# Kernel optimization log

Measured on AMD Instinct MI355X. Metric: run time of the kernel, lower is better.

## Reference

```python
import jax, jax.numpy as jnp
import numpy as np

B, S, D, H, DFF = 4, 2048, 1024, 16, 4096
HD = D // H  # head_dim = 64


def rmsnorm(x, scale, eps=1e-6):
    var = jnp.mean(jnp.square(x), axis=-1, keepdims=True)
    return x * jax.lax.rsqrt(var + eps) * scale


def setup_inputs() -> dict:
    key = jax.random.key(0)
    ks = jax.random.split(key, 16)
    s = 1.0 / np.sqrt(D)
    inp = {
        "x": jax.random.normal(ks[0], (B, S, D), jnp.float32),
        "wq": jax.random.normal(ks[1], (D, D), jnp.float32) * s,
        "bq": jnp.zeros((D,), jnp.float32),
        "wk": jax.random.normal(ks[2], (D, D), jnp.float32) * s,
        "bk": jnp.zeros((D,), jnp.float32),
        "wv": jax.random.normal(ks[3], (D, D), jnp.float32) * s,
        "bv": jnp.zeros((D,), jnp.float32),
        "wbeta": jax.random.normal(ks[4], (D, H), jnp.float32) * s,
        "bbeta": jnp.zeros((H,), jnp.float32),
        "wo": jax.random.normal(ks[5], (D, D), jnp.float32) * s,
        "bo": jnp.zeros((D,), jnp.float32),
        "w1": jax.random.normal(ks[6], (D, DFF), jnp.float32) * s,
        "b1": jnp.zeros((DFF,), jnp.float32),
        "w2": jax.random.normal(ks[7], (DFF, D), jnp.float32) * (1.0 / np.sqrt(DFF)),
        "b2": jnp.zeros((D,), jnp.float32),
        "ln1_scale": jnp.ones((D,), jnp.float32),
        "ln2_scale": jnp.ones((D,), jnp.float32),
    }
    return inp


def gdn_attention(x, wq, bq, wk, bk, wv, bv, wbeta, bbeta, wo, bo):
    b, s, _ = x.shape
    q = (x @ wq + bq).reshape(b, s, H, HD)
    k = (x @ wk + bk).reshape(b, s, H, HD)
    v = (x @ wv + bv).reshape(b, s, H, HD)
    k = k / (jnp.linalg.norm(k, axis=-1, keepdims=True) + 1e-6)
    beta = jax.nn.sigmoid(x @ wbeta + bbeta)[..., None]  # (b, s, H, 1)

    # time-major for scan: (s, b, H, ...)
    q = jnp.transpose(q, (1, 0, 2, 3))
    k = jnp.transpose(k, (1, 0, 2, 3))
    v = jnp.transpose(v, (1, 0, 2, 3))
    beta = jnp.transpose(beta, (1, 0, 2, 3))

    def _step(Sm, inputs):
        q_t, k_t, v_t, beta_t = inputs
        Sk = jnp.einsum('bhde,bhe->bhd', Sm, k_t)
        delta = v_t - Sk
        Sm = Sm + beta_t[..., None] * jnp.einsum('bhd,bhe->bhde', delta, k_t)
        o_t = jnp.einsum('bhde,bhe->bhd', Sm, q_t)
        return Sm, o_t

    S0 = jnp.zeros((b, H, HD, HD), x.dtype)
    _, outputs = jax.lax.scan(_step, S0, (q, k, v, beta))
    outputs = jnp.transpose(outputs, (1, 0, 2, 3)).reshape(b, s, D)
    return outputs @ wo + bo


def reference(x, wq, bq, wk, bk, wv, bv, wbeta, bbeta, wo, bo,
              w1, b1, w2, b2, ln1_scale, ln2_scale):
    residual = x
    h = rmsnorm(x, ln1_scale)
    h = gdn_attention(h, wq, bq, wk, bk, wv, bv, wbeta, bbeta, wo, bo)
    x = h + residual
    residual = x
    h = rmsnorm(x, ln2_scale)
    h = jax.nn.gelu(h @ w1 + b1) @ w2 + b2
    return h + residual
```

## Files before the change

kernel.cpp:

```cpp
#include <hip/hip_runtime.h>

#define DEV __device__ __forceinline__

typedef short bf16x8 __attribute__((ext_vector_type(8)));
typedef float f32x4 __attribute__((ext_vector_type(4)));
typedef unsigned int uint;

DEV unsigned short f2b(float f) {
    uint u = __float_as_uint(f);
    u += 0x7fffu + ((u >> 16) & 1u);
    return (unsigned short)(u >> 16);
}
DEV uint packbf2(float a, float b) { return (uint)f2b(a) | ((uint)f2b(b) << 16); }
DEV float b2f(unsigned short s) { return __uint_as_float(((uint)s) << 16); }
DEV float b2f_lo(uint u) { return __uint_as_float(u << 16); }
DEV float b2f_hi(uint u) { return __uint_as_float(u & 0xffff0000u); }

DEV void async_cp16(const void* g, void* l) {
    __builtin_amdgcn_global_load_lds(
        (const __attribute__((address_space(1))) unsigned int*)g,
        (__attribute__((address_space(3))) unsigned int*)l, 16, 0, 0);
}

DEV float quad_sum(float x) {
    x += __int_as_float(__builtin_amdgcn_update_dpp(0, __float_as_int(x), 0xB1, 0xF, 0xF, true));
    x += __int_as_float(__builtin_amdgcn_update_dpp(0, __float_as_int(x), 0x4E, 0xF, 0xF, true));
    return x;
}

DEV float gelu_f(float u) {
    float p = u + 0.044715f * u * u * u;
    float e = __expf(-1.5957691216f * p);
    return __fdividef(u, 1.f + e);
}

DEV void dec8(uint4 p, float* o) {
    o[0] = b2f_lo(p.x); o[1] = b2f_hi(p.x); o[2] = b2f_lo(p.y); o[3] = b2f_hi(p.y);
    o[4] = b2f_lo(p.z); o[5] = b2f_hi(p.z); o[6] = b2f_lo(p.w); o[7] = b2f_hi(p.w);
}

__global__ __launch_bounds__(256) void transpose_cast_k(
    const float* __restrict__ in, unsigned short* __restrict__ out, int K, int N)
{
    __shared__ float tile[32][33];
    const int k0 = blockIdx.x * 32, n0 = blockIdx.y * 32;
    const int tx = threadIdx.x & 31, ty = threadIdx.x >> 5;
#pragma unroll
    for (int i = 0; i < 32; i += 8) {
        int n = n0 + tx;
        tile[ty + i][tx] = (n < N) ? in[(size_t)(k0 + ty + i) * N + n] : 0.0f;
    }
    __syncthreads();
#pragma unroll
    for (int i = 0; i < 32; i += 8) {
        out[(size_t)(n0 + ty + i) * K + (k0 + tx)] = f2b(tile[tx][ty + i]);
    }
}

__global__ void build_bias_k(const float* __restrict__ bq, const float* __restrict__ bk,
                             const float* __restrict__ bv, const float* __restrict__ bb,
                             float* __restrict__ outb)
{
    int i = blockIdx.x * 256 + threadIdx.x;
    if (i >= 3328) return;
    float v = 0.f;
    if (i < 1024)      v = bq[i];
    else if (i < 2048) v = bk[i - 1024];
    else if (i < 3072) v = bv[i - 2048];
    else if (i < 3088) v = bb[i - 3072];
    outb[i] = v;
}

__global__ __launch_bounds__(256) void rmsnorm_cast_k(
    const float* __restrict__ x, const float* __restrict__ scale,
    unsigned short* __restrict__ out)
{
    const int row = blockIdx.x;
    const int t = threadIdx.x;
    const float4 v = *(const float4*)(x + (size_t)row * 1024 + t * 4);
    float ss = v.x * v.x + v.y * v.y + v.z * v.z + v.w * v.w;
#pragma unroll
    for (int off = 1; off < 64; off <<= 1) ss += __shfl_xor(ss, off);
    __shared__ float wsum[4];
    if ((t & 63) == 0) wsum[t >> 6] = ss;
    __syncthreads();
    const float tot = wsum[0] + wsum[1] + wsum[2] + wsum[3];
    const float inv = rsqrtf(tot * (1.0f / 1024.0f) + 1e-6f);
    const float4 sc = *(const float4*)(scale + t * 4);
    uint lo = (uint)f2b(v.x * inv * sc.x) | ((uint)f2b(v.y * inv * sc.y) << 16);
    uint hi = (uint)f2b(v.z * inv * sc.z) | ((uint)f2b(v.w * inv * sc.w) << 16);
    uint2 pkd; pkd.x = lo; pkd.y = hi;
    *(uint2*)(out + (size_t)row * 1024 + t * 4) = pkd;
}

template <bool GELU, bool GUARD>
__global__ __launch_bounds__(512, 2) void gemm256(
    const unsigned short* __restrict__ A, const unsigned short* __restrict__ BT,
    const float* __restrict__ bias, unsigned short* __restrict__ C,
    int Nstride, int Nreal, int K)
{
    __shared__ __align__(16) unsigned short As[4][256 * 32];
    __shared__ __align__(16) unsigned short Bs[4][256 * 32];
    const int tid = threadIdx.x;
    const int wid = tid >> 6;
    const int lane = tid & 63;
    const int l16 = lane & 15, quad = lane >> 4;
    const int wm = wid & 1, wn = wid >> 1;
    const int m0 = blockIdx.x << 8, n0 = blockIdx.y << 8;

    const int srow = (wid << 5) + (lane >> 2);
    const int scol = (lane & 3) << 3;
    const unsigned short* Ag = A + (size_t)(m0 + srow) * K + scol;
    const unsigned short* Bg = BT + (size_t)(n0 + srow) * K + scol;
    const size_t rstep16 = (size_t)16 * K;
    const int ldst = wid << 10;

    f32x4 acc[8][4];
#pragma unroll
    for (int i = 0; i < 8; i++)
#pragma unroll
        for (int j = 0; j < 4; j++) acc[i][j] = (f32x4)0.f;

    const int aoff = ((wm << 7) + l16) * 32 + (quad << 3);
    const int boff = ((wn << 6) + l16) * 32 + (quad << 3);

    const int nt = K >> 5;
    async_cp16(Ag, &As[0][ldst]);
    async_cp16(Ag + rstep16, &As[0][ldst + 512]);
    async_cp16(Bg, &Bs[0][ldst]);
    async_cp16(Bg + rstep16, &Bs[0][ldst + 512]);
    async_cp16(Ag + 32, &As[1][ldst]);
    async_cp16(Ag + 32 + rstep16, &As[1][ldst + 512]);
    async_cp16(Bg + 32, &Bs[1][ldst]);
    async_cp16(Bg + 32 + rstep16, &Bs[1][ldst + 512]);
    asm volatile("s_waitcnt vmcnt(4)" ::: "memory");
    __builtin_amdgcn_s_barrier();

    for (int tb = 0; tb < nt; tb += 4) {
#pragma unroll
        for (int u = 0; u < 4; ++u) {
            const int t = tb + u;
            const int pb = (u + 2) & 3;
            const bool st = (t + 2) < nt;
            const size_t kpre = (size_t)(t + 2) << 5;
            bf16x8 af[4], bfr[4];
#pragma unroll
            for (int mi = 0; mi < 4; mi++) af[mi] = *(const bf16x8*)&As[u][aoff + mi * 512];
#pragma unroll
            for (int ni = 0; ni < 4; ni++) bfr[ni] = *(const bf16x8*)&Bs[u][boff + ni * 512];
            if (st) {
                async_cp16(Ag + kpre, &As[pb][ldst]);
                async_cp16(Ag + kpre + rstep16, &As[pb][ldst + 512]);
            }
            __builtin_amdgcn_s_barrier();
            asm volatile("s_waitcnt lgkmcnt(0)" ::: "memory");
            __builtin_amdgcn_s_setprio(1);
#pragma unroll
            for (int mi = 0; mi < 4; mi++)
#pragma unroll
                for (int ni = 0; ni < 4; ni++)
                    acc[mi][ni] = __builtin_amdgcn_mfma_f32_16x16x32_bf16(af[mi], bfr[ni], acc[mi][ni], 0, 0, 0);
            __builtin_amdgcn_s_setprio(0);
            __builtin_amdgcn_s_barrier();
#pragma unroll
            for (int mi = 0; mi < 4; mi++) af[mi] = *(const bf16x8*)&As[u][aoff + (mi + 4) * 512];
            if (st) {
                async_cp16(Bg + kpre, &Bs[pb][ldst]);
                async_cp16(Bg + kpre + rstep16, &Bs[pb][ldst + 512]);
            }
            asm volatile("s_waitcnt vmcnt(4)" ::: "memory");
            __builtin_amdgcn_s_barrier();
            asm volatile("s_waitcnt lgkmcnt(0)" ::: "memory");
            __builtin_amdgcn_s_setprio(1);
#pragma unroll
            for (int mi = 0; mi < 4; mi++)
#pragma unroll
                for (int ni = 0; ni < 4; ni++)
                    acc[mi + 4][ni] = __builtin_amdgcn_mfma_f32_16x16x32_bf16(af[mi], bfr[ni], acc[mi + 4][ni], 0, 0, 0);
            __builtin_amdgcn_s_setprio(0);
            __builtin_amdgcn_s_barrier();
        }
    }

    float bv[4];
    const int ccol = n0 + (wn << 6) + l16;
#pragma unroll
    for (int ni = 0; ni < 4; ni++) bv[ni] = bias[ccol + ni * 16];
#pragma unroll
    for (int mi = 0; mi < 8; mi++) {
        const int row = m0 + (wm << 7) + mi * 16 + (quad << 2);
#pragma unroll
        for (int r = 0; r < 4; r++) {
            unsigned short* Crow = C + (size_t)(row + r) * Nstride + ccol;
#pragma unroll
            for (int ni = 0; ni < 4; ni++) {
                float v = acc[mi][ni][r] + bv[ni];
                if (GELU) v = gelu_f(v);
                if (!GUARD || (ccol + ni * 16) < Nreal) Crow[ni * 16] = f2b(v);
            }
        }
    }
}

template <int MODE>
__global__ __launch_bounds__(256) void gemm_bt(
    const unsigned short* __restrict__ A, const unsigned short* __restrict__ BT,
    const float* __restrict__ bias, const float* __restrict__ add,
    void* __restrict__ Cout, int N, int K)
{
    __shared__ unsigned short As[128 * 32];
    __shared__ unsigned short Bs[128 * 32];
    const int tid = threadIdx.x;
    const int wid = tid >> 6;
    const int lane = tid & 63;
    const int m0 = blockIdx.x * 128;
    const int n0 = blockIdx.y * 128;

    const int lrow = lane >> 2;
    const int lkw = (((lane & 3) ^ ((lane >> 3) & 3))) * 8;

    const unsigned short* Ag0 = A + (size_t)(m0 + wid * 16 + lrow) * K + lkw;
    const unsigned short* Ag1 = A + (size_t)(m0 + wid * 16 + 64 + lrow) * K + lkw;
    const unsigned short* Bg0 = BT + (size_t)(n0 + wid * 16 + lrow) * K + lkw;
    const unsigned short* Bg1 = BT + (size_t)(n0 + wid * 16 + 64 + lrow) * K + lkw;
    unsigned short* As0 = &As[(wid * 16) * 32];
    unsigned short* As1 = &As[(wid * 16 + 64) * 32];
    unsigned short* Bs0 = &Bs[(wid * 16) * 32];
    unsigned short* Bs1 = &Bs[(wid * 16 + 64) * 32];

    f32x4 acc[4][4];
#pragma unroll
    for (int i = 0; i < 4; i++)
#pragma unroll
        for (int j = 0; j < 4; j++) acc[i][j] = (f32x4)0.f;

    const int wm = (wid & 1) * 64;
    const int wn = (wid >> 1) * 64;
    const int l16 = lane & 15;
    const int quad = lane >> 4;
    const int koffs = (quad ^ ((l16 >> 1) & 3)) * 8;

    for (int k0 = 0; k0 < K; k0 += 32) {
        async_cp16(Ag0 + k0, As0);
        async_cp16(Ag1 + k0, As1);
        async_cp16(Bg0 + k0, Bs0);
        async_cp16(Bg1 + k0, Bs1);
        __syncthreads();
        bf16x8 af[4], bfv[4];
#pragma unroll
        for (int i = 0; i < 4; i++) af[i] = *(const bf16x8*)&As[(wm + i * 16 + l16) * 32 + koffs];
#pragma unroll
        for (int j = 0; j < 4; j++) bfv[j] = *(const bf16x8*)&Bs[(wn + j * 16 + l16) * 32 + koffs];
#pragma unroll
        for (int i = 0; i < 4; i++)
#pragma unroll
            for (int j = 0; j < 4; j++)
                acc[i][j] = __builtin_amdgcn_mfma_f32_16x16x32_bf16(af[i], bfv[j], acc[i][j], 0, 0, 0);
        __syncthreads();
    }

    if (MODE == 2 || MODE == 3) {
        float* ep = ((wid & 2) ? (float*)Bs : (float*)As) + (wid & 1) * 1024;
        const int rr = lane >> 2, cg = lane & 3;
        unsigned short* Cu = (unsigned short*)Cout;
#pragma unroll
        for (int i = 0; i < 4; i++) {
#pragma unroll
            for (int p = 0; p < 2; p++) {
#pragma unroll
                for (int jj = 0; jj < 2; jj++) {
                    const int j = 2 * p + jj;
                    const float bv = bias[n0 + wn + j * 16 + l16];
#pragma unroll
                    for (int r = 0; r < 4; r++) {
                        float v = acc[i][j][r] + bv;
                        if (MODE == 2) v = gelu_f(v);
                        ep[(jj * 16 + l16) * 17 + quad * 4 + r] = v;
                    }
                }
                __syncthreads();
                uint4 pk;
                float f[8];
#pragma unroll
                for (int m = 0; m < 8; m++) f[m] = ep[(cg * 8 + m) * 17 + rr];
                pk.x = packbf2(f[0], f[1]); pk.y = packbf2(f[2], f[3]);
                pk.z = packbf2(f[4], f[5]); pk.w = packbf2(f[6], f[7]);
                *(uint4*)(Cu + (size_t)(m0 + wm + i * 16 + rr) * N + (n0 + wn + p * 32 + cg * 8)) = pk;
                __syncthreads();
            }
        }
    } else {
#pragma unroll
        for (int j = 0; j < 4; j++) {
            const int cg2 = n0 + wn + j * 16 + l16;
            const float bv = bias[cg2];
#pragma unroll
            for (int i = 0; i < 4; i++) {
                const int rg0 = m0 + wm + i * 16 + quad * 4;
#pragma unroll
                for (int r = 0; r < 4; r++) {
                    size_t idx = (size_t)(rg0 + r) * N + cg2;
                    float v = acc[i][j][r] + bv;
                    if (MODE == 1) v += add[idx];
                    ((float*)Cout)[idx] = v;
                }
            }
        }
    }
}


__global__ __launch_bounds__(256) void gdn_prep(
    unsigned short* __restrict__ qkv, unsigned short* __restrict__ Wg,
    unsigned short* __restrict__ ZTg, unsigned short* __restrict__ KTg)
{
    const int chunk = blockIdx.x, bh = blockIdx.y;
    const int b = bh >> 4, h = bh & 15;
    __shared__ float Ks[64 * 68];
    __shared__ float Ws[64 * 65];
    __shared__ float Zs[64 * 65];
    __shared__ float Asl[64 * 65];
    __shared__ float bs[64];
    const int tid = threadIdx.x;
    const int t = tid >> 2, c = tid & 3;
    unsigned short* rowp = qkv + (size_t)(b * 2048 + chunk * 64 + t) * 3200;

    float kn[16];
    {
        uint4 ka = *(const uint4*)(rowp + 1024 + h * 64 + 16 * c);
        uint4 kb = *(const uint4*)(rowp + 1024 + h * 64 + 16 * c + 8);
        dec8(ka, kn); dec8(kb, kn + 8);
    }
    float ss = 0.f;
#pragma unroll
    for (int j = 0; j < 16; j++) ss += kn[j] * kn[j];
    ss = quad_sum(ss);
    const float inv = 1.f / (sqrtf(ss) + 1e-6f);
#pragma unroll
    for (int j = 0; j < 16; j++) kn[j] *= inv;
#pragma unroll
    for (int j = 0; j < 16; j++) Ks[t * 68 + 16 * c + j] = kn[j];
    {
        uint4 p0, p1;
        p0.x = packbf2(kn[0], kn[1]);  p0.y = packbf2(kn[2], kn[3]);
        p0.z = packbf2(kn[4], kn[5]);  p0.w = packbf2(kn[6], kn[7]);
        p1.x = packbf2(kn[8], kn[9]);  p1.y = packbf2(kn[10], kn[11]);
        p1.z = packbf2(kn[12], kn[13]); p1.w = packbf2(kn[14], kn[15]);
        *(uint4*)(rowp + 1024 + h * 64 + 16 * c) = p0;
        *(uint4*)(rowp + 1024 + h * 64 + 16 * c + 8) = p1;
    }
    if (c == 0) bs[t] = 1.f / (1.f + __expf(-b2f(rowp[3072 + h])));
    __syncthreads();

    const float beta = bs[t];
#pragma unroll
    for (int j = 0; j < 16; j++) Ws[t * 65 + 16 * c + j] = beta * kn[j];
    {
        float vv[16];
        uint4 va = *(const uint4*)(rowp + 2048 + h * 64 + 16 * c);
        uint4 vb = *(const uint4*)(rowp + 2048 + h * 64 + 16 * c + 8);
        dec8(va, vv); dec8(vb, vv + 8);
#pragma unroll
        for (int j = 0; j < 16; j++) Zs[t * 65 + 16 * c + j] = beta * vv[j];
    }
    __syncthreads();

    {
        const int tt = tid >> 4, sx = tid & 15;
        float dm[4][4];
#pragma unroll
        for (int i = 0; i < 4; i++)
#pragma unroll
            for (int j = 0; j < 4; j++) dm[i][j] = 0.f;
        for (int d = 0; d < 64; d++) {
            float kt[4], ksv[4];
#pragma unroll
            for (int i = 0; i < 4; i++) kt[i] = Ks[(4 * tt + i) * 68 + d];
#pragma unroll
            for (int j = 0; j < 4; j++) ksv[j] = Ks[(4 * sx + j) * 68 + d];
#pragma unroll
            for (int i = 0; i < 4; i++)
#pragma unroll
                for (int j = 0; j < 4; j++) dm[i][j] += kt[i] * ksv[j];
        }
#pragma unroll
        for (int i = 0; i < 4; i++)
#pragma unroll
            for (int j = 0; j < 4; j++) {
                int T = 4 * tt + i, S_ = 4 * sx + j;
                Asl[T * 65 + S_] = (S_ < T) ? bs[T] * dm[i][j] : 0.f;
            }
    }
    __syncthreads();

    {
        const int wid = tid >> 6, lane = tid & 63;
        for (int qi = 0; qi < 4; qi++) {
            if (qi > 0) {
                const int tb = qi * 16 + wid * 4;
                float aw[4], az[4];
#pragma unroll
                for (int i = 0; i < 4; i++) { aw[i] = Ws[(tb + i) * 65 + lane]; az[i] = Zs[(tb + i) * 65 + lane]; }
                for (int s = 0; s < qi * 16; s++) {
                    float wsv = Ws[s * 65 + lane], zsv = Zs[s * 65 + lane];
#pragma unroll
                    for (int i = 0; i < 4; i++) {
                        float a = Asl[(tb + i) * 65 + s];
                        aw[i] -= a * wsv; az[i] -= a * zsv;
                    }
                }
#pragma unroll
                for (int i = 0; i < 4; i++) { Ws[(tb + i) * 65 + lane] = aw[i]; Zs[(tb + i) * 65 + lane] = az[i]; }
            }
            __syncthreads();
            if (wid == 0) {
                for (int T = qi * 16; T < qi * 16 + 16; T++) {
                    float a_ = Ws[T * 65 + lane];
                    for (int s = qi * 16; s < T; s++) a_ -= Asl[T * 65 + s] * Ws[s * 65 + lane];
                    Ws[T * 65 + lane] = a_;
                }
            } else if (wid == 1) {
                for (int T = qi * 16; T < qi * 16 + 16; T++) {
                    float a_ = Zs[T * 65 + lane];
                    for (int s = qi * 16; s < T; s++) a_ -= Asl[T * 65 + s] * Zs[s * 65 + lane];
                    Zs[T * 65 + lane] = a_;
                }
            }
            __syncthreads();
        }
    }

    const size_t cbase = ((size_t)bh * 32 + chunk) * 4096;
    {
#pragma unroll
        for (int half = 0; half < 2; half++) {
            uint4 w4;
            w4.x = packbf2(Ws[t * 65 + 16 * c + half * 8 + 0], Ws[t * 65 + 16 * c + half * 8 + 1]);
            w4.y = packbf2(Ws[t * 65 + 16 * c + half * 8 + 2], Ws[t * 65 + 16 * c + half * 8 + 3]);
            w4.z = packbf2(Ws[t * 65 + 16 * c + half * 8 + 4], Ws[t * 65 + 16 * c + half * 8 + 5]);
            w4.w = packbf2(Ws[t * 65 + 16 * c + half * 8 + 6], Ws[t * 65 + 16 * c + half * 8 + 7]);
            *(uint4*)(Wg + cbase + (size_t)((2 * c + half) * 64 + t) * 8) = w4;
        }
    }
    {
        const int jj = tid >> 2, tq = tid & 3;
#pragma unroll
        for (int half = 0; half < 2; half++) {
            uint4 z4;
            int i0 = half * 8;
            z4.x = packbf2(Zs[(16 * tq + i0 + 0) * 65 + jj], Zs[(16 * tq + i0 + 1) * 65 + jj]);
            z4.y = packbf2(Zs[(16 * tq + i0 + 2) * 65 + jj], Zs[(16 * tq + i0 + 3) * 65 + jj]);
            z4.z = packbf2(Zs[(16 * tq + i0 + 4) * 65 + jj], Zs[(16 * tq + i0 + 5) * 65 + jj]);
            z4.w = packbf2(Zs[(16 * tq + i0 + 6) * 65 + jj], Zs[(16 * tq + i0 + 7) * 65 + jj]);
            *(uint4*)(ZTg + cbase + (size_t)((2 * tq + half) * 64 + jj) * 8) = z4;
        }
    }
    {
        const int dd = tid >> 2, tq = tid & 3;
#pragma unroll
        for (int half = 0; half < 2; half++) {
            uint4 k4;
            int i0 = half * 8;
            k4.x = packbf2(Ks[(16 * tq + i0 + 0) * 68 + dd], Ks[(16 * tq + i0 + 1) * 68 + dd]);
            k4.y = packbf2(Ks[(16 * tq + i0 + 2) * 68 + dd], Ks[(16 * tq + i0 + 3) * 68 + dd]);
            k4.z = packbf2(Ks[(16 * tq + i0 + 4) * 68 + dd], Ks[(16 * tq + i0 + 5) * 68 + dd]);
            k4.w = packbf2(Ks[(16 * tq + i0 + 6) * 68 + dd], Ks[(16 * tq + i0 + 7) * 68 + dd]);
            *(uint4*)(KTg + cbase + (size_t)((2 * tq + half) * 64 + dd) * 8) = k4;
        }
    }
}

__global__ __launch_bounds__(256, 1) void gdn_prop_mfma(
    const unsigned short* __restrict__ Wg, const unsigned short* __restrict__ KTg,
    const unsigned short* __restrict__ ZTg, unsigned short* __restrict__ Sall,
    unsigned short* __restrict__ Yg)
{
    const int bh = blockIdx.x;
    __shared__ unsigned short WbU[4096];
    __shared__ unsigned short KTbU[4096];
    __shared__ unsigned short ZTbU[4096];
    __shared__ unsigned short SbU[4096];
    const int tid = threadIdx.x;
    const int wid = tid >> 6;
    const int lane = tid & 63;
    const int l16 = lane & 15, quad = lane >> 4;

    f32x4 Sacc[4];
#pragma unroll
    for (int dt = 0; dt < 4; dt++) Sacc[dt] = (f32x4)0.f;

    for (int ch = 0; ch < 32; ch++) {
        const size_t cbase = ((size_t)bh * 32 + ch) * 4096;
#pragma unroll
        for (int p = 0; p < 2; p++) {
            const int n = wid * 2 + p;
            async_cp16(Wg + cbase + n * 512 + lane * 8, &WbU[n * 512]);
            async_cp16(KTg + cbase + n * 512 + lane * 8, &KTbU[n * 512]);
            async_cp16(ZTg + cbase + n * 512 + lane * 8, &ZTbU[n * 512]);
        }
#pragma unroll
        for (int dt = 0; dt < 4; dt++) {
#pragma unroll
            for (int r = 0; r < 4; r++) {
                const int j = wid * 16 + quad * 4 + r;
                SbU[((2 * dt + (l16 >> 3)) * 64 + j) * 8 + (l16 & 7)] = f2b(Sacc[dt][r]);
            }
            const int d = dt * 16 + l16;
            uint2 sp;
            sp.x = packbf2(Sacc[dt][0], Sacc[dt][1]);
            sp.y = packbf2(Sacc[dt][2], Sacc[dt][3]);
            *(uint2*)(Sall + cbase + d * 64 + wid * 16 + quad * 4) = sp;
        }
        __syncthreads();

        f32x4 t1[4];
#pragma unroll
        for (int tt = 0; tt < 4; tt++) t1[tt] = (f32x4)0.f;
#pragma unroll
        for (int kh = 0; kh < 2; kh++) {
            const int g = kh * 4 + quad;
            bf16x8 afr = *(const bf16x8*)&SbU[(g * 64 + wid * 16 + l16) * 8];
#pragma unroll
            for (int tt = 0; tt < 4; tt++) {
                bf16x8 bfr = *(const bf16x8*)&WbU[(g * 64 + tt * 16 + l16) * 8];
                t1[tt] = __builtin_amdgcn_mfma_f32_16x16x32_bf16(afr, bfr, t1[tt], 0, 0, 0);
            }
        }
#pragma unroll
        for (int tt = 0; tt < 4; tt++) {
            const int t = tt * 16 + l16;
            const int gb = (t >> 3) * 64;
            unsigned short ybf[4];
#pragma unroll
            for (int r = 0; r < 4; r++) {
                const int j = wid * 16 + quad * 4 + r;
                const float z = b2f(ZTbU[(gb + j) * 8 + (t & 7)]);
                ybf[r] = f2b(z - t1[tt][r]);
            }
#pragma unroll
            for (int r = 0; r < 4; r++) {
                const int j = wid * 16 + quad * 4 + r;
                ZTbU[(gb + j) * 8 + (t & 7)] = ybf[r];
            }
            uint2 yp;
            yp.x = (uint)ybf[0] | ((uint)ybf[1] << 16);
            yp.y = (uint)ybf[2] | ((uint)ybf[3] << 16);
            *(uint2*)(Yg + cbase + t * 64 + wid * 16 + quad * 4) = yp;
        }
#pragma unroll
        for (int kh = 0; kh < 2; kh++) {
            const int g = kh * 4 + quad;
            bf16x8 afr = *(const bf16x8*)&ZTbU[(g * 64 + wid * 16 + l16) * 8];
#pragma unroll
            for (int dt = 0; dt < 4; dt++) {
                bf16x8 bfr = *(const bf16x8*)&KTbU[(g * 64 + dt * 16 + l16) * 8];
                Sacc[dt] = __builtin_amdgcn_mfma_f32_16x16x32_bf16(afr, bfr, Sacc[dt], 0, 0, 0);
            }
        }
        __syncthreads();
    }
}

__global__ __launch_bounds__(256) void gdn_out(
    const unsigned short* __restrict__ qkv, const unsigned short* __restrict__ Yg,
    const unsigned short* __restrict__ Sall, unsigned short* __restrict__ attn)
{
    const int chunk = blockIdx.x, bh = blockIdx.y;
    const int b = bh >> 4, h = bh & 15;
    __shared__ float Qf[64 * 68];
    __shared__ float SfT[64 * 68];
    __shared__ float Ms[64 * 65];
    __shared__ uint Kp[64 * 33];
    __shared__ uint Yp[64 * 34];
    const int tid = threadIdx.x;
    const int t = tid >> 2, c = tid & 3;
    const size_t cbase = ((size_t)bh * 32 + chunk) * 4096;

    {
        const unsigned short* rowp = qkv + (size_t)(b * 2048 + chunk * 64 + t) * 3200;
        float qv[16];
        uint4 qa = *(const uint4*)(rowp + h * 64 + 16 * c);
        uint4 qb = *(const uint4*)(rowp + h * 64 + 16 * c + 8);
        dec8(qa, qv); dec8(qb, qv + 8);
#pragma unroll
        for (int m = 0; m < 16; m++) Qf[t * 68 + 16 * c + m] = qv[m];
        uint4 ka = *(const uint4*)(rowp + 1024 + h * 64 + 16 * c);
        uint4 kb = *(const uint4*)(rowp + 1024 + h * 64 + 16 * c + 8);
        Kp[t * 33 + 8 * c + 0] = ka.x; Kp[t * 33 + 8 * c + 1] = ka.y;
        Kp[t * 33 + 8 * c + 2] = ka.z; Kp[t * 33 + 8 * c + 3] = ka.w;
        Kp[t * 33 + 8 * c + 4] = kb.x; Kp[t * 33 + 8 * c + 5] = kb.y;
        Kp[t * 33 + 8 * c + 6] = kb.z; Kp[t * 33 + 8 * c + 7] = kb.w;
        const unsigned short* yrow = Yg + cbase + t * 64 + 16 * c;
        uint4 ya = *(const uint4*)yrow;
        uint4 yb = *(const uint4*)(yrow + 8);
        Yp[t * 34 + 8 * c + 0] = ya.x; Yp[t * 34 + 8 * c + 1] = ya.y;
        Yp[t * 34 + 8 * c + 2] = ya.z; Yp[t * 34 + 8 * c + 3] = ya.w;
        Yp[t * 34 + 8 * c + 4] = yb.x; Yp[t * 34 + 8 * c + 5] = yb.y;
        Yp[t * 34 + 8 * c + 6] = yb.z; Yp[t * 34 + 8 * c + 7] = yb.w;
        const unsigned short* srow = Sall + cbase + t * 64 + 16 * c;
        float sv[16];
        uint4 sa = *(const uint4*)srow;
        uint4 sb = *(const uint4*)(srow + 8);
        dec8(sa, sv); dec8(sb, sv + 8);
#pragma unroll
        for (int m = 0; m < 16; m++) SfT[t * 68 + 16 * c + m] = sv[m];
    }
    __syncthreads();

    const int tt = tid >> 4, sx = tid & 15;
    {
        float dm[4][4];
#pragma unroll
        for (int i = 0; i < 4; i++)
#pragma unroll
            for (int j = 0; j < 4; j++) dm[i][j] = 0.f;
        for (int p = 0; p < 32; p++) {
            float q0[4], q1[4];
#pragma unroll
            for (int i = 0; i < 4; i++) {
                q0[i] = Qf[(4 * tt + i) * 68 + 2 * p];
                q1[i] = Qf[(4 * tt + i) * 68 + 2 * p + 1];
            }
#pragma unroll
            for (int j = 0; j < 4; j++) {
                uint kp = Kp[(4 * sx + j) * 33 + p];
                float kk0 = b2f_lo(kp), kk1 = b2f_hi(kp);
#pragma unroll
                for (int i = 0; i < 4; i++) dm[i][j] += q0[i] * kk0 + q1[i] * kk1;
            }
        }
#pragma unroll
        for (int i = 0; i < 4; i++)
#pragma unroll
            for (int j = 0; j < 4; j++) {
                int T = 4 * tt + i, S_ = 4 * sx + j;
                Ms[T * 65 + S_] = (S_ <= T) ? dm[i][j] : 0.f;
            }
    }
    __syncthreads();

    {
        float o[4][4];
#pragma unroll
        for (int i = 0; i < 4; i++)
#pragma unroll
            for (int j = 0; j < 4; j++) o[i][j] = 0.f;
        for (int d = 0; d < 64; d++) {
            float qv[4];
#pragma unroll
            for (int i = 0; i < 4; i++) qv[i] = Qf[(4 * tt + i) * 68 + d];
#pragma unroll
            for (int j = 0; j < 4; j++) {
                float sv = SfT[d * 68 + 4 * sx + j];
#pragma unroll
                for (int i = 0; i < 4; i++) o[i][j] += qv[i] * sv;
            }
        }
        for (int s = 0; s < 64; s++) {
            float mv[4];
#pragma unroll
            for (int i = 0; i < 4; i++) mv[i] = Ms[(4 * tt + i) * 65 + s];
            uint2 yp2 = *(const uint2*)&Yp[s * 34 + 2 * sx];
            float yv0 = b2f_lo(yp2.x), yv1 = b2f_hi(yp2.x), yv2 = b2f_lo(yp2.y), yv3 = b2f_hi(yp2.y);
#pragma unroll
            for (int i = 0; i < 4; i++) {
                o[i][0] += mv[i] * yv0; o[i][1] += mv[i] * yv1;
                o[i][2] += mv[i] * yv2; o[i][3] += mv[i] * yv3;
            }
        }
#pragma unroll
        for (int i = 0; i < 4; i++) {
            uint2 op; op.x = packbf2(o[i][0], o[i][1]); op.y = packbf2(o[i][2], o[i][3]);
            *(uint2*)(attn + (size_t)(b * 2048 + chunk * 64 + 4 * tt + i) * 1024 + h * 64 + 4 * sx) = op;
        }
    }
}

static constexpr size_t OFF_H     = 0;
static constexpr size_t OFF_WQKVT = OFF_H + 16777216;
static constexpr size_t OFF_WOT   = OFF_WQKVT + 6553600;
static constexpr size_t OFF_W1T   = OFF_WOT + 2097152;
static constexpr size_t OFF_W2T   = OFF_W1T + 8388608;
static constexpr size_t OFF_BIAS  = OFF_W2T + 8388608;
static constexpr size_t OFF_QKV   = OFF_BIAS + 16384;
static constexpr size_t OFF_ATTN  = OFF_QKV + 67108864;
static constexpr size_t OFF_Y1    = OFF_ATTN + 16777216;
static constexpr size_t OFF_WG    = OFF_Y1 + 33554432;
static constexpr size_t OFF_YG    = OFF_WG + 16777216;

extern "C" void kernel_launch(void* const* d_in, const int* in_sizes, int n_in,
                              void* d_out, int out_size, void* d_ws, size_t ws_size,
                              hipStream_t stream)
{
    const float* x     = (const float*)d_in[0];
    const float* wq    = (const float*)d_in[1];
    const float* bq    = (const float*)d_in[2];
    const float* wk    = (const float*)d_in[3];
    const float* bk    = (const float*)d_in[4];
    const float* wv    = (const float*)d_in[5];
    const float* bv    = (const float*)d_in[6];
    const float* wbeta = (const float*)d_in[7];
    const float* bbeta = (const float*)d_in[8];
    const float* wo    = (const float*)d_in[9];
    const float* bo    = (const float*)d_in[10];
    const float* w1    = (const float*)d_in[11];
    const float* b1    = (const float*)d_in[12];
    const float* w2    = (const float*)d_in[13];
    const float* b2    = (const float*)d_in[14];
    const float* ln1   = (const float*)d_in[15];
    const float* ln2   = (const float*)d_in[16];

    char* ws = (char*)d_ws;
    unsigned short* hbuf  = (unsigned short*)(ws + OFF_H);
    unsigned short* Sall  = (unsigned short*)(ws + OFF_H);
    unsigned short* wqkvT = (unsigned short*)(ws + OFF_WG);
    unsigned short* woT   = (unsigned short*)(ws + OFF_WOT);
    unsigned short* w1T   = (unsigned short*)(ws + OFF_W1T);
    unsigned short* w2T   = (unsigned short*)(ws + OFF_W2T);
    float*          biasc = (float*)(ws + OFF_BIAS);
    unsigned short* qkvU  = (unsigned short*)(ws + OFF_QKV);
    unsigned short* gbuf  = (unsigned short*)(ws + OFF_QKV);
    unsigned short* attn  = (unsigned short*)(ws + OFF_ATTN);
    float*          y1    = (float*)(ws + OFF_Y1);
    unsigned short* ZTg   = (unsigned short*)(ws + OFF_Y1);
    unsigned short* KTg   = (unsigned short*)(ws + OFF_Y1 + 16777216);
    unsigned short* Wg    = (unsigned short*)(ws + OFF_WG);
    unsigned short* Yg    = (unsigned short*)(ws + OFF_YG);
    float*          out   = (float*)d_out;

    transpose_cast_k<<<dim3(32, 32), 256, 0, stream>>>(wq, wqkvT,               1024, 1024);
    transpose_cast_k<<<dim3(32, 32), 256, 0, stream>>>(wk, wqkvT + 1024 * 1024, 1024, 1024);
    transpose_cast_k<<<dim3(32, 32), 256, 0, stream>>>(wv, wqkvT + 2048 * 1024, 1024, 1024);
    transpose_cast_k<<<dim3(32, 8),  256, 0, stream>>>(wbeta, wqkvT + 3072 * 1024, 1024, 16);
    transpose_cast_k<<<dim3(32, 32), 256, 0, stream>>>(wo, woT, 1024, 1024);
    transpose_cast_k<<<dim3(32, 128), 256, 0, stream>>>(w1, w1T, 1024, 4096);
    transpose_cast_k<<<dim3(128, 32), 256, 0, stream>>>(w2, w2T, 4096, 1024);
    build_bias_k<<<13, 256, 0, stream>>>(bq, bk, bv, bbeta, biasc);

    rmsnorm_cast_k<<<8192, 256, 0, stream>>>(x, ln1, hbuf);
    gemm256<false, true><<<dim3(32, 13), 512, 0, stream>>>(hbuf, wqkvT, biasc, qkvU, 3200, 3200, 1024);
    gdn_prep<<<dim3(32, 64), 256, 0, stream>>>(qkvU, Wg, ZTg, KTg);
    gdn_prop_mfma<<<64, 256, 0, stream>>>(Wg, KTg, ZTg, Sall, Yg);
    gdn_out<<<dim3(32, 64), 256, 0, stream>>>(qkvU, Yg, Sall, attn);
    gemm_bt<1><<<dim3(64, 8), 256, 0, stream>>>(attn, woT, bo, x, y1, 1024, 1024);
    rmsnorm_cast_k<<<8192, 256, 0, stream>>>(y1, ln2, hbuf);
    gemm256<true, false><<<dim3(32, 16), 512, 0, stream>>>(hbuf, w1T, b1, gbuf, 4096, 4096, 1024);
    gemm_bt<1><<<dim3(64, 8), 256, 0, stream>>>(gbuf, w2T, b2, y1, out, 1024, 4096);
}
```

Baseline: 684.3 us.

## Replace gemm_bt with pipelined 128x256 GEMM and swizzle gemm256 LDS

The single-buffered 128x128 gemm_bt used for the output projection and FFN down-projection is replaced by a new 512-thread 128x256 kernel. It uses a 4-stage async global-to-LDS pipeline with prefetch two tiles ahead, fewer barriers, and raised wave priority around the MFMAs. gemm256 gains an XOR swizzle of the LDS K offset to reduce bank conflicts, and its last iterations now drain outstanding loads with vmcnt(0). The aim is to overlap memory with MFMA and improve reuse in the two K-heavy fp32-output GEMMs, at the cost of more LDS and a smaller grid of 256 blocks.

```diff
diff --git a/kernel.cpp b/kernel.cpp
--- a/kernel.cpp
+++ b/kernel.cpp
@@ -5,6 +5,10 @@
 typedef short bf16x8 __attribute__((ext_vector_type(8)));
 typedef float f32x4 __attribute__((ext_vector_type(4)));
 typedef unsigned int uint;
+
+#define SBAR()   asm volatile("s_barrier" ::: "memory")
+#define WAITV(n) asm volatile("s_waitcnt vmcnt(" #n ")" ::: "memory")
+#define WAITL()  asm volatile("s_waitcnt lgkmcnt(0)" ::: "memory")
 
 DEV unsigned short f2b(float f) {
     uint u = __float_as_uint(f);
@@ -109,7 +113,7 @@
     const int m0 = blockIdx.x << 8, n0 = blockIdx.y << 8;
 
     const int srow = (wid << 5) + (lane >> 2);
-    const int scol = (lane & 3) << 3;
+    const int scol = ((lane & 3) ^ ((lane >> 3) & 3)) << 3;
     const unsigned short* Ag = A + (size_t)(m0 + srow) * K + scol;
     const unsigned short* Bg = BT + (size_t)(n0 + srow) * K + scol;
     const size_t rstep16 = (size_t)16 * K;
@@ -121,8 +125,9 @@
 #pragma unroll
         for (int j = 0; j < 4; j++) acc[i][j] = (f32x4)0.f;
 
-    const int aoff = ((wm << 7) + l16) * 32 + (quad << 3);
-    const int boff = ((wn << 6) + l16) * 32 + (quad << 3);
+    const int ksw = (quad ^ ((l16 >> 1) & 3)) << 3;
+    const int aoff = ((wm << 7) + l16) * 32 + ksw;
+    const int boff = ((wn << 6) + l16) * 32 + ksw;
 
     const int nt = K >> 5;
     async_cp16(Ag, &As[0][ldst]);
@@ -133,8 +138,8 @@
     async_cp16(Ag + 32 + rstep16, &As[1][ldst + 512]);
     async_cp16(Bg + 32, &Bs[1][ldst]);
     async_cp16(Bg + 32 + rstep16, &Bs[1][ldst + 512]);
-    asm volatile("s_waitcnt vmcnt(4)" ::: "memory");
-    __builtin_amdgcn_s_barrier();
+    WAITV(4);
+    SBAR();
 
     for (int tb = 0; tb < nt; tb += 4) {
 #pragma unroll
@@ -152,8 +157,8 @@
                 async_cp16(Ag + kpre, &As[pb][ldst]);
                 async_cp16(Ag + kpre + rstep16, &As[pb][ldst + 512]);
             }
-            __builtin_amdgcn_s_barrier();
-            asm volatile("s_waitcnt lgkmcnt(0)" ::: "memory");
+            SBAR();
+            WAITL();
             __builtin_amdgcn_s_setprio(1);
 #pragma unroll
             for (int mi = 0; mi < 4; mi++)
@@ -161,16 +166,18 @@
                 for (int ni = 0; ni < 4; ni++)
                     acc[mi][ni] = __builtin_amdgcn_mfma_f32_16x16x32_bf16(af[mi], bfr[ni], acc[mi][ni], 0, 0, 0);
             __builtin_amdgcn_s_setprio(0);
-            __builtin_amdgcn_s_barrier();
+            SBAR();
 #pragma unroll
             for (int mi = 0; mi < 4; mi++) af[mi] = *(const bf16x8*)&As[u][aoff + (mi + 4) * 512];
             if (st) {
                 async_cp16(Bg + kpre, &Bs[pb][ldst]);
                 async_cp16(Bg + kpre + rstep16, &Bs[pb][ldst + 512]);
-            }
-            asm volatile("s_waitcnt vmcnt(4)" ::: "memory");
-            __builtin_amdgcn_s_barrier();
-            asm volatile("s_waitcnt lgkmcnt(0)" ::: "memory");
+                WAITV(4);
+            } else {
+                WAITV(0);
+            }
+            SBAR();
+            WAITL();
             __builtin_amdgcn_s_setprio(1);
 #pragma unroll
             for (int mi = 0; mi < 4; mi++)
@@ -178,7 +185,7 @@
                 for (int ni = 0; ni < 4; ni++)
                     acc[mi + 4][ni] = __builtin_amdgcn_mfma_f32_16x16x32_bf16(af[mi], bfr[ni], acc[mi + 4][ni], 0, 0, 0);
             __builtin_amdgcn_s_setprio(0);
-            __builtin_amdgcn_s_barrier();
+            SBAR();
         }
     }
 
@@ -202,31 +209,29 @@
     }
 }
 
-template <int MODE>
-__global__ __launch_bounds__(256) void gemm_bt(
+template <bool ADD>
+__global__ __launch_bounds__(512, 2) void gemm128n256(
     const unsigned short* __restrict__ A, const unsigned short* __restrict__ BT,
     const float* __restrict__ bias, const float* __restrict__ add,
-    void* __restrict__ Cout, int N, int K)
-{
-    __shared__ unsigned short As[128 * 32];
-    __shared__ unsigned short Bs[128 * 32];
+    float* __restrict__ C, int N, int K)
+{
+    __shared__ __align__(16) unsigned short As[4][128 * 32];
+    __shared__ __align__(16) unsigned short Bs[4][256 * 32];
     const int tid = threadIdx.x;
     const int wid = tid >> 6;
     const int lane = tid & 63;
-    const int m0 = blockIdx.x * 128;
-    const int n0 = blockIdx.y * 128;
-
-    const int lrow = lane >> 2;
-    const int lkw = (((lane & 3) ^ ((lane >> 3) & 3))) * 8;
-
-    const unsigned short* Ag0 = A + (size_t)(m0 + wid * 16 + lrow) * K + lkw;
-    const unsigned short* Ag1 = A + (size_t)(m0 + wid * 16 + 64 + lrow) * K + lkw;
-    const unsigned short* Bg0 = BT + (size_t)(n0 + wid * 16 + lrow) * K + lkw;
-    const unsigned short* Bg1 = BT + (size_t)(n0 + wid * 16 + 64 + lrow) * K + lkw;
-    unsigned short* As0 = &As[(wid * 16) * 32];
-    unsigned short* As1 = &As[(wid * 16 + 64) * 32];
-    unsigned short* Bs0 = &Bs[(wid * 16) * 32];
-    unsigned short* Bs1 = &Bs[(wid * 16 + 64) * 32];
+    const int l16 = lane & 15, quad = lane >> 4;
+    const int wm = wid & 1, wn = wid >> 1;
+    const int m0 = blockIdx.x << 7, n0 = blockIdx.y << 8;
+
+    const int arow = (wid << 4) + (lane >> 2);
+    const int brow = (wid << 5) + (lane >> 2);
+    const int scol = ((lane & 3) ^ ((lane >> 3) & 3)) << 3;
+    const unsigned short* Ag = A + (size_t)(m0 + arow) * K + scol;
+    const unsigned short* Bg = BT + (size_t)(n0 + brow) * K + scol;
+    const size_t rstep16 = (size_t)16 * K;
+    const int lda = wid << 9;
+    const int ldb = wid << 10;
 
     f32x4 acc[4][4];
 #pragma unroll
@@ -234,76 +239,66 @@
 #pragma unroll
         for (int j = 0; j < 4; j++) acc[i][j] = (f32x4)0.f;
 
-    const int wm = (wid & 1) * 64;
-    const int wn = (wid >> 1) * 64;
-    const int l16 = lane & 15;
-    const int quad = lane >> 4;
-    const int koffs = (quad ^ ((l16 >> 1) & 3)) * 8;
-
-    for (int k0 = 0; k0 < K; k0 += 32) {
-        async_cp16(Ag0 + k0, As0);
-        async_cp16(Ag1 + k0, As1);
-        async_cp16(Bg0 + k0, Bs0);
-        async_cp16(Bg1 + k0, Bs1);
-        __syncthreads();
-        bf16x8 af[4], bfv[4];
-#pragma unroll
-        for (int i = 0; i < 4; i++) af[i] = *(const bf16x8*)&As[(wm + i * 16 + l16) * 32 + koffs];
-#pragma unroll
-        for (int j = 0; j < 4; j++) bfv[j] = *(const bf16x8*)&Bs[(wn + j * 16 + l16) * 32 + koffs];
-#pragma unroll
-        for (int i = 0; i < 4; i++)
-#pragma unroll
-            for (int j = 0; j < 4; j++)
-                acc[i][j] = __builtin_amdgcn_mfma_f32_16x16x32_bf16(af[i], bfv[j], acc[i][j], 0, 0, 0);
-        __syncthreads();
-    }
-
-    if (MODE == 2 || MODE == 3) {
-        float* ep = ((wid & 2) ? (float*)Bs : (float*)As) + (wid & 1) * 1024;
-        const int rr = lane >> 2, cg = lane & 3;
-        unsigned short* Cu = (unsigned short*)Cout;
-#pragma unroll
-        for (int i = 0; i < 4; i++) {
-#pragma unroll
-            for (int p = 0; p < 2; p++) {
-#pragma unroll
-                for (int jj = 0; jj < 2; jj++) {
-                    const int j = 2 * p + jj;
-                    const float bv = bias[n0 + wn + j * 16 + l16];
-#pragma unroll
-                    for (int r = 0; r < 4; r++) {
-                        float v = acc[i][j][r] + bv;
-                        if (MODE == 2) v = gelu_f(v);
-                        ep[(jj * 16 + l16) * 17 + quad * 4 + r] = v;
-                    }
-                }
-                __syncthreads();
-                uint4 pk;
-                float f[8];
-#pragma unroll
-                for (int m = 0; m < 8; m++) f[m] = ep[(cg * 8 + m) * 17 + rr];
-                pk.x = packbf2(f[0], f[1]); pk.y = packbf2(f[2], f[3]);
-                pk.z = packbf2(f[4], f[5]); pk.w = packbf2(f[6], f[7]);
-                *(uint4*)(Cu + (size_t)(m0 + wm + i * 16 + rr) * N + (n0 + wn + p * 32 + cg * 8)) = pk;
-                __syncthreads();
-            }
-        }
-    } else {
-#pragma unroll
-        for (int j = 0; j < 4; j++) {
-            const int cg2 = n0 + wn + j * 16 + l16;
-            const float bv = bias[cg2];
-#pragma unroll
-            for (int i = 0; i < 4; i++) {
-                const int rg0 = m0 + wm + i * 16 + quad * 4;
-#pragma unroll
-                for (int r = 0; r < 4; r++) {
-                    size_t idx = (size_t)(rg0 + r) * N + cg2;
-                    float v = acc[i][j][r] + bv;
-                    if (MODE == 1) v += add[idx];
-                    ((float*)Cout)[idx] = v;
-                }
+    const int ksw = (quad ^ ((l16 >> 1) & 3)) << 3;
+    const int aoff = ((wm << 6) + l16) * 32 + ksw;
+    const int boff = ((wn << 6) + l16) * 32 + ksw;
+
+    const int nt = K >> 5;
+    async_cp16(Ag, &As[0][lda]);
+    async_cp16(Bg, &Bs[0][ldb]);
+    async_cp16(Bg + rstep16, &Bs[0][ldb + 512]);
+    async_cp16(Ag + 32, &As[1][lda]);
+    async_cp16(Bg + 32, &Bs[1][ldb]);
+    async_cp16(Bg + 32 + rstep16, &Bs[1][ldb + 512]);
+    WAITV(3);
+    SBAR();
+
+    for (int tb = 0; tb < nt; tb += 4) {
+#pragma unroll
+        for (int u = 0; u < 4; ++u) {
+            const int t = tb + u;
+            const int pb = (u + 2) & 3;
+            const bool st = (t + 2) < nt;
+            const size_t kpre = (size_t)(t + 2) << 5;
+            bf16x8 af[4], bfr[4];
+#pragma unroll
+            for (int mi = 0; mi < 4; mi++) af[mi] = *(const bf16x8*)&As[u][aoff + mi * 512];
+#pragma unroll
+            for (int ni = 0; ni < 4; ni++) bfr[ni] = *(const bf16x8*)&Bs[u][boff + ni * 512];
+            if (st) {
+                async_cp16(Ag + kpre, &As[pb][lda]);
+                async_cp16(Bg + kpre, &Bs[pb][ldb]);
+                async_cp16(Bg + kpre + rstep16, &Bs[pb][ldb + 512]);
+            }
+            SBAR();
+            WAITL();
+            __builtin_amdgcn_s_setprio(1);
+#pragma unroll
+            for (int mi = 0; mi < 4; mi++)
+#pragma unroll
+                for (int ni = 0; ni < 4; ni++)
+                    acc[mi][ni] = __builtin_amdgcn_mfma_f32_16x16x32_bf16(af[mi], bfr[ni], acc[mi][ni], 0, 0, 0);
+            __builtin_amdgcn_s_setprio(0);
+            if (st) { WAITV(3); } else { WAITV(0); }
+            SBAR();
+        }
+    }
+
+    const int ccol = n0 + (wn << 6) + l16;
+    float bv[4];
+#pragma unroll
+    for (int ni = 0; ni < 4; ni++) bv[ni] = bias[ccol + ni * 16];
+#pragma unroll
+    for (int mi = 0; mi < 4; mi++) {
+        const int row = m0 + (wm << 6) + mi * 16 + (quad << 2);
+#pragma unroll
+        for (int r = 0; r < 4; r++) {
+#pragma unroll
+            for (int ni = 0; ni < 4; ni++) {
+                size_t idx = (size_t)(row + r) * N + ccol + ni * 16;
+                float v = acc[mi][ni][r] + bv[ni];
+                if (ADD) v += add[idx];
+                C[idx] = v;
             }
         }
     }
@@ -742,8 +737,8 @@
     gdn_prep<<<dim3(32, 64), 256, 0, stream>>>(qkvU, Wg, ZTg, KTg);
     gdn_prop_mfma<<<64, 256, 0, stream>>>(Wg, KTg, ZTg, Sall, Yg);
     gdn_out<<<dim3(32, 64), 256, 0, stream>>>(qkvU, Yg, Sall, attn);
-    gemm_bt<1><<<dim3(64, 8), 256, 0, stream>>>(attn, woT, bo, x, y1, 1024, 1024);
+    gemm128n256<true><<<dim3(64, 4), 512, 0, stream>>>(attn, woT, bo, x, y1, 1024, 1024);
     rmsnorm_cast_k<<<8192, 256, 0, stream>>>(y1, ln2, hbuf);
     gemm256<true, false><<<dim3(32, 16), 512, 0, stream>>>(hbuf, w1T, b1, gbuf, 4096, 4096, 1024);
-    gemm_bt<1><<<dim3(64, 8), 256, 0, stream>>>(gbuf, w2T, b2, y1, out, 1024, 4096);
-}
+    gemm128n256<true><<<dim3(64, 4), 512, 0, stream>>>(gbuf, w2T, b2, y1, out, 1024, 4096);
+}
```

Measured after the change: 653.9 us. 4.4% less time.
